# Optimization experiments

Measured on AMD Instinct MI355X. Metric: run time of the kernel, lower is better.

Reference implementation:

```python
import jax, jax.numpy as jnp
import numpy as np

N, E, IN, K, F, D = 50000, 800000, 256, 4, 64, 2


def setup_inputs() -> dict:
    key = jax.random.key(0)
    ks = jax.random.split(key, 10)
    # CSR rowptr: 0 .. E, nondecreasing, endpoints pinned
    inner = jnp.sort(jax.random.randint(ks[0], (N - 1,), 0, E + 1))
    rowptr = jnp.concatenate([jnp.zeros(1, jnp.int64), inner.astype(jnp.int64), jnp.full(1, E, jnp.int64)])
    colind = jax.random.randint(ks[1], (E,), 0, N).astype(jnp.int64)
    # CSC mirrors (used only by the fused kernel's backward; inert in forward math)
    inner_c = jnp.sort(jax.random.randint(ks[2], (N - 1,), 0, E + 1))
    colptr = jnp.concatenate([jnp.zeros(1, jnp.int64), inner_c.astype(jnp.int64), jnp.full(1, E, jnp.int64)])
    rowind = jax.random.randint(ks[3], (E,), 0, N).astype(jnp.int64)
    permute = jnp.arange(E, dtype=jnp.int64)
    feat = jax.random.normal(ks[4], (N, IN), dtype=jnp.float32)
    pseudo = jax.random.uniform(ks[5], (E, D), dtype=jnp.float32)
    # params: fc weight [K*F, IN] (xavier-normal style scale), mu ~ N(0, 0.1), inv_sigma = 1, bias = 0
    gain = float(np.sqrt(2.0))
    std = gain * float(np.sqrt(2.0 / (IN + K * F)))
    W_fc = jax.random.normal(ks[6], (K * F, IN), dtype=jnp.float32) * std
    mu = jax.random.normal(ks[7], (K, D), dtype=jnp.float32) * 0.1
    inv_sigma = jnp.ones((K, D), dtype=jnp.float32)
    bias = jnp.zeros((F,), dtype=jnp.float32)
    return {"rowptr": rowptr, "colind": colind, "colptr": colptr, "rowind": rowind,
            "permute": permute, "feat": feat, "pseudo": pseudo,
            "W_fc": W_fc, "mu": mu, "inv_sigma": inv_sigma, "bias": bias}


def reference(rowptr, colind, colptr, rowind, permute, feat, pseudo, W_fc, mu, inv_sigma, bias):
    n = feat.shape[0]
    e = colind.shape[0]
    k, d = mu.shape
    f = W_fc.shape[0] // k
    # dense projection: [N, K, F]
    node_feat = (feat @ W_fc.T).reshape(n, k, f)
    # per-edge Gaussian mixture weights: [E, K]
    diff = pseudo[:, None, :] - mu[None, :, :]              # [E, K, D]
    gaussian = jnp.exp(jnp.sum(-0.5 * diff * diff * (inv_sigma[None, :, :] ** 2), axis=-1))
    # multi-head SpMM: gather source feats, weight per kernel, sum kernels (sum commutes
    # with the segment reduction, so fold the head-sum into the edge message): [E, F]
    msg = jnp.einsum('ek,ekf->ef', gaussian, node_feat[colind])
    # destination node of each CSR edge
    dst = jnp.searchsorted(rowptr, jnp.arange(e), side='right') - 1
    rst = jax.ops.segment_sum(msg, dst, num_segments=n)      # [N, F]
    return rst + bias
```

## Files before the change

### kernel.cpp

```cpp
#include <hip/hip_runtime.h>


typedef _Float16 f16;
typedef __attribute__((ext_vector_type(2))) _Float16 f16x2;
typedef __attribute__((ext_vector_type(4))) _Float16 f16x4;
typedef __attribute__((ext_vector_type(8))) _Float16 f16x8;
typedef __attribute__((ext_vector_type(4))) float f32x4;

__device__ inline f16x4 cvt4h(float4 v) {
    f16x4 h;
    h.x = (f16)v.x; h.y = (f16)v.y; h.z = (f16)v.z; h.w = (f16)v.w;
    return h;
}

__global__ __launch_bounds__(256) void convert_W(
    const float* __restrict__ W, f16* __restrict__ Wp)
{
    const int gid = blockIdx.x * 256 + threadIdx.x;
    const int jp = gid >> 6, k4 = gid & 63;
    const int wrow = ((jp & 3) << 6) | (jp >> 2);
    reinterpret_cast<f16x4*>(Wp)[jp * 64 + k4] =
        cvt4h(reinterpret_cast<const float4*>(W)[wrow * 64 + k4]);
}

#define ASTRIDE 264

__global__ __launch_bounds__(256) void gemm_fused(
    const float* __restrict__ feat,
    const f16* __restrict__ Wp,
    f16* __restrict__ nf,
    int M)
{
    __shared__ f16 As[64 * ASTRIDE];
    __shared__ f16 Bs[256 * 32];
    const int t    = threadIdx.x;
    const int lane = t & 63;
    const int wave = t >> 6;
    const int bm   = blockIdx.x * 64;
    const int l16  = lane & 15;
    const int quad = lane >> 4;
    const int wn   = wave * 64;

    size_t bsrc[4];
#pragma unroll
    for (int j = 0; j < 4; ++j)
        bsrc[j] = (size_t)(wave * 64 + j * 16 + (lane >> 2)) * 256 + (lane & 3) * 8;

    typedef __attribute__((address_space(3))) void lds_t;
    typedef const __attribute__((address_space(1))) void gm_t;

#pragma unroll
    for (int j = 0; j < 4; ++j)
        __builtin_amdgcn_global_load_lds((gm_t*)(Wp + bsrc[j]),
            (lds_t*)(Bs + (wave * 4 + j) * 512), 16, 0, 0);

#pragma unroll
    for (int it = 0; it < 8; ++it) {
        const int flat = it * 2048 + t * 8;
        const int row  = flat >> 8;
        const int koff = flat & 255;
        const float* src = feat + (size_t)min(bm + row, M - 1) * 256 + koff;
        const float4 a0 = *reinterpret_cast<const float4*>(src);
        const float4 a1 = *reinterpret_cast<const float4*>(src + 4);
        *reinterpret_cast<f16x4*>(&As[row * ASTRIDE + koff])     = cvt4h(a0);
        *reinterpret_cast<f16x4*>(&As[row * ASTRIDE + koff + 4]) = cvt4h(a1);
    }

    f32x4 acc[4][4];
#pragma unroll
    for (int mi = 0; mi < 4; ++mi)
#pragma unroll
        for (int ni = 0; ni < 4; ++ni)
            acc[mi][ni] = (f32x4){0.f, 0.f, 0.f, 0.f};

    for (int ki = 0; ki < 8; ++ki) {
        __syncthreads();

        f16x8 af[4], bfr[4];
#pragma unroll
        for (int mi = 0; mi < 4; ++mi)
            af[mi] = *reinterpret_cast<const f16x8*>(
                &As[(mi * 16 + l16) * ASTRIDE + ki * 32 + quad * 8]);
#pragma unroll
        for (int ni = 0; ni < 4; ++ni)
            bfr[ni] = *reinterpret_cast<const f16x8*>(
                &Bs[(wn + ni * 16 + l16) * 32 + quad * 8]);

        __syncthreads();
        if (ki < 7) {
            const int k0 = (ki + 1) * 32;
#pragma unroll
            for (int j = 0; j < 4; ++j)
                __builtin_amdgcn_global_load_lds((gm_t*)(Wp + bsrc[j] + k0),
                    (lds_t*)(Bs + (wave * 4 + j) * 512), 16, 0, 0);
        }
#pragma unroll
        for (int mi = 0; mi < 4; ++mi)
#pragma unroll
            for (int ni = 0; ni < 4; ++ni)
                acc[mi][ni] = __builtin_amdgcn_mfma_f32_16x16x32_f16(
                    af[mi], bfr[ni], acc[mi][ni], 0, 0, 0);
    }

#pragma unroll
    for (int mi = 0; mi < 4; ++mi) {
#pragma unroll
        for (int r = 0; r < 4; ++r) {
            const int row = bm + mi * 16 + quad * 4 + r;
            if (row < M) {
#pragma unroll
                for (int ni = 0; ni < 4; ++ni) {
                    const int col = wn + ni * 16 + l16;
                    nf[(size_t)row * 256 + col] = (f16)(acc[mi][ni][r]);
                }
            }
        }
    }
}

__global__ __launch_bounds__(128) void edge_aggregate(
    const int* __restrict__ rowptr,
    const int* __restrict__ colind,
    const float* __restrict__ pseudo,
    const f16* __restrict__ nf,
    const float* __restrict__ mu,
    const float* __restrict__ inv_sigma,
    const float* __restrict__ bias,
    float* __restrict__ out,
    int N)
{
    __shared__ f16 gbuf[2][64];
    __shared__ int cbuf[2][16];
    const int wave = threadIdx.x >> 6;
    const int lane = threadIdx.x & 63;
    const int node = blockIdx.x * 2 + wave;
    if (node >= N) return;

    const int kk = lane >> 4;
    const int ii = lane & 15;
    const float mx = mu[2 * kk], my = mu[2 * kk + 1];
    const float sa = inv_sigma[2 * kk], sb = inv_sigma[2 * kk + 1];
    const float sx = sa * sa, sy = sb * sb;

    const int e0 = rowptr[node];
    const int e1 = rowptr[node + 1];
    f16* gw = gbuf[wave];
    int* cw = cbuf[wave];

    float a4[4] = {0.f, 0.f, 0.f, 0.f};
    for (int ec = e0; ec < e1; ec += 16) {
        const int cnt = min(16, e1 - ec);
        {
            const bool v = ii < cnt;
            const int e = v ? (ec + ii) : e0;
            const float2 p = *reinterpret_cast<const float2*>(pseudo + 2 * (size_t)e);
            const float dx = p.x - mx, dy = p.y - my;
            const float g = v ? __expf(-0.5f * (dx * dx * sx + dy * dy * sy)) : 0.f;
            gw[ii * 4 + kk] = (f16)g;
            if (kk == 0) cw[ii] = v ? colind[e] : 0;
        }
        __builtin_amdgcn_wave_barrier();
        __threadfence_block();
        const int cnt4 = (cnt + 3) & ~3;
        for (int i2 = 0; i2 < cnt4; i2 += 4) {
#pragma unroll
            for (int j = 0; j < 4; ++j) {
                const int c = cw[i2 + j];
                const f16x4 h = *reinterpret_cast<const f16x4*>(
                    nf + ((size_t)c << 8) + (lane << 2));
                const f16x2 g01 = *reinterpret_cast<const f16x2*>(&gw[(i2 + j) * 4]);
                const f16x2 g23 = *reinterpret_cast<const f16x2*>(&gw[(i2 + j) * 4 + 2]);
                const f16x2 h01 = __builtin_shufflevector(h, h, 0, 1);
                const f16x2 h23 = __builtin_shufflevector(h, h, 2, 3);
#if __has_builtin(__builtin_amdgcn_fdot2)
                a4[j] = __builtin_amdgcn_fdot2(h01, g01, a4[j], false);
                a4[j] = __builtin_amdgcn_fdot2(h23, g23, a4[j], false);
#else
                a4[j] += (float)h01.x * (float)g01.x + (float)h01.y * (float)g01.y
                       + (float)h23.x * (float)g23.x + (float)h23.y * (float)g23.y;
#endif
            }
        }
        __builtin_amdgcn_wave_barrier();
        __threadfence_block();
    }
    out[((size_t)node << 6) + lane] =
        (a4[0] + a4[1]) + (a4[2] + a4[3]) + bias[lane];
}

extern "C" void kernel_launch(void* const* d_in, const int* in_sizes, int n_in,
                              void* d_out, int out_size, void* d_ws, size_t ws_size,
                              hipStream_t stream)
{
    const int*   rowptr    = (const int*)d_in[0];
    const int*   colind    = (const int*)d_in[1];
    const float* feat      = (const float*)d_in[5];
    const float* pseudo    = (const float*)d_in[6];
    const float* W_fc      = (const float*)d_in[7];
    const float* mu        = (const float*)d_in[8];
    const float* inv_sigma = (const float*)d_in[9];
    const float* bias      = (const float*)d_in[10];
    float* out = (float*)d_out;

    const int N = in_sizes[0] - 1;
    f16* nf = (f16*)d_ws;
    f16* Wp = (f16*)d_out;

    hipLaunchKernelGGL(convert_W, dim3(64), dim3(256), 0, stream, W_fc, Wp);

    hipLaunchKernelGGL(gemm_fused, dim3((N + 63) / 64), dim3(256), 0, stream,
                       feat, Wp, nf, N);

    hipLaunchKernelGGL(edge_aggregate, dim3((N + 1) / 2), dim3(128), 0, stream,
                       rowptr, colind, pseudo, nf, mu, inv_sigma, bias, out, N);
}
```

Before: 189.6 us.

## Quantize projected node features and gaussian weights to int8 with per-row scales

The GEMM epilogue now quantizes each node's projected features to int8 with one scale per row and per head, staging the result through shared memory for coalesced stores. The edge aggregation gathers int8 rows plus scales and uses an int8 dot4 against gaussian weights quantized to int8. The goal is to halve the gather bytes in the memory-bound SpMM phase. In exchange it loses accuracy and adds a scale load per edge.

```diff
diff --git a/kernel.cpp b/kernel.cpp
--- a/kernel.cpp
+++ b/kernel.cpp
@@ -2,7 +2,6 @@
 
 
 typedef _Float16 f16;
-typedef __attribute__((ext_vector_type(2))) _Float16 f16x2;
 typedef __attribute__((ext_vector_type(4))) _Float16 f16x4;
 typedef __attribute__((ext_vector_type(8))) _Float16 f16x8;
 typedef __attribute__((ext_vector_type(4))) float f32x4;
@@ -11,6 +10,17 @@
     f16x4 h;
     h.x = (f16)v.x; h.y = (f16)v.y; h.z = (f16)v.z; h.w = (f16)v.w;
     return h;
+}
+
+__device__ inline int dot4_i8(int a, int b) {
+#if __has_builtin(__builtin_amdgcn_sdot4)
+    return __builtin_amdgcn_sdot4(a, b, 0, false);
+#else
+    return (int)(char)(a)       * (int)(char)(b)
+         + (int)(char)(a >> 8)  * (int)(char)(b >> 8)
+         + (int)(char)(a >> 16) * (int)(char)(b >> 16)
+         + (int)(char)(a >> 24) * (int)(char)(b >> 24);
+#endif
 }
 
 __global__ __launch_bounds__(256) void convert_W(
@@ -24,15 +34,19 @@
 }
 
 #define ASTRIDE 264
+#define AS_BYTES (64 * ASTRIDE * 2)
 
 __global__ __launch_bounds__(256) void gemm_fused(
     const float* __restrict__ feat,
     const f16* __restrict__ Wp,
-    f16* __restrict__ nf,
+    char* __restrict__ nfq,
+    float* __restrict__ sc,
     int M)
 {
-    __shared__ f16 As[64 * ASTRIDE];
-    __shared__ f16 Bs[256 * 32];
+    __shared__ char smem[AS_BYTES + 256 * 32 * 2];
+    f16* As = (f16*)smem;
+    f16* Bs = (f16*)(smem + AS_BYTES);
+    char* qt = smem + AS_BYTES;
     const int t    = threadIdx.x;
     const int lane = t & 63;
     const int wave = t >> 6;
@@ -106,14 +120,37 @@
     for (int mi = 0; mi < 4; ++mi) {
 #pragma unroll
         for (int r = 0; r < 4; ++r) {
-            const int row = bm + mi * 16 + quad * 4 + r;
-            if (row < M) {
-#pragma unroll
-                for (int ni = 0; ni < 4; ++ni) {
-                    const int col = wn + ni * 16 + l16;
-                    nf[(size_t)row * 256 + col] = (f16)(acc[mi][ni][r]);
-                }
+            float am = 0.f;
+#pragma unroll
+            for (int ni = 0; ni < 4; ++ni)
+                am = fmaxf(am, fabsf(acc[mi][ni][r]));
+            am = fmaxf(am, __shfl_xor(am, 1));
+            am = fmaxf(am, __shfl_xor(am, 2));
+            am = fmaxf(am, __shfl_xor(am, 4));
+            am = fmaxf(am, __shfl_xor(am, 8));
+            const float sinv = am > 0.f ? 127.f / am : 0.f;
+            const int rl = mi * 16 + quad * 4 + r;
+#pragma unroll
+            for (int ni = 0; ni < 4; ++ni)
+                qt[rl * 256 + wn + ni * 16 + l16] =
+                    (char)(int)__builtin_rintf(acc[mi][ni][r] * sinv);
+            if (l16 == 0) {
+                const int row = bm + rl;
+                if (row < M) sc[row * 4 + wave] = am * (1.f / 16129.f);
             }
+        }
+    }
+    __syncthreads();
+
+    {
+        const int rl  = t >> 2;
+        const int co  = (t & 3) * 64;
+        const int row = bm + rl;
+        if (row < M) {
+            const int4* s4 = reinterpret_cast<const int4*>(qt + rl * 256 + co);
+            int4* d4 = reinterpret_cast<int4*>(nfq + (size_t)row * 256 + co);
+#pragma unroll
+            for (int j = 0; j < 4; ++j) d4[j] = s4[j];
         }
     }
 }
@@ -122,14 +159,15 @@
     const int* __restrict__ rowptr,
     const int* __restrict__ colind,
     const float* __restrict__ pseudo,
-    const f16* __restrict__ nf,
+    const char* __restrict__ nfq,
+    const float* __restrict__ sc,
     const float* __restrict__ mu,
     const float* __restrict__ inv_sigma,
     const float* __restrict__ bias,
     float* __restrict__ out,
     int N)
 {
-    __shared__ f16 gbuf[2][64];
+    __shared__ int gpack[2][16];
     __shared__ int cbuf[2][16];
     const int wave = threadIdx.x >> 6;
     const int lane = threadIdx.x & 63;
@@ -144,7 +182,7 @@
 
     const int e0 = rowptr[node];
     const int e1 = rowptr[node + 1];
-    f16* gw = gbuf[wave];
+    int* gp = gpack[wave];
     int* cw = cbuf[wave];
 
     float a4[4] = {0.f, 0.f, 0.f, 0.f};
@@ -156,7 +194,7 @@
             const float2 p = *reinterpret_cast<const float2*>(pseudo + 2 * (size_t)e);
             const float dx = p.x - mx, dy = p.y - my;
             const float g = v ? __expf(-0.5f * (dx * dx * sx + dy * dy * sy)) : 0.f;
-            gw[ii * 4 + kk] = (f16)g;
+            ((char*)&gp[ii])[kk] = (char)(int)(g * 127.f + 0.5f);
             if (kk == 0) cw[ii] = v ? colind[e] : 0;
         }
         __builtin_amdgcn_wave_barrier();
@@ -166,19 +204,11 @@
 #pragma unroll
             for (int j = 0; j < 4; ++j) {
                 const int c = cw[i2 + j];
-                const f16x4 h = *reinterpret_cast<const f16x4*>(
-                    nf + ((size_t)c << 8) + (lane << 2));
-                const f16x2 g01 = *reinterpret_cast<const f16x2*>(&gw[(i2 + j) * 4]);
-                const f16x2 g23 = *reinterpret_cast<const f16x2*>(&gw[(i2 + j) * 4 + 2]);
-                const f16x2 h01 = __builtin_shufflevector(h, h, 0, 1);
-                const f16x2 h23 = __builtin_shufflevector(h, h, 2, 3);
-#if __has_builtin(__builtin_amdgcn_fdot2)
-                a4[j] = __builtin_amdgcn_fdot2(h01, g01, a4[j], false);
-                a4[j] = __builtin_amdgcn_fdot2(h23, g23, a4[j], false);
-#else
-                a4[j] += (float)h01.x * (float)g01.x + (float)h01.y * (float)g01.y
-                       + (float)h23.x * (float)g23.x + (float)h23.y * (float)g23.y;
-#endif
+                const int q = *reinterpret_cast<const int*>(
+                    nfq + ((size_t)c << 8) + (lane << 2));
+                const float s = sc[c * 4 + (lane >> 4)];
+                const int d = dot4_i8(q, gp[i2 + j]);
+                a4[j] += s * (float)d;
             }
         }
         __builtin_amdgcn_wave_barrier();
@@ -203,14 +233,15 @@
     float* out = (float*)d_out;
 
     const int N = in_sizes[0] - 1;
-    f16* nf = (f16*)d_ws;
-    f16* Wp = (f16*)d_out;
+    char*  nfq = (char*)d_ws;
+    float* sc  = (float*)(nfq + (size_t)N * 256);
+    f16*   Wp  = (f16*)d_out;
 
     hipLaunchKernelGGL(convert_W, dim3(64), dim3(256), 0, stream, W_fc, Wp);
 
     hipLaunchKernelGGL(gemm_fused, dim3((N + 63) / 64), dim3(256), 0, stream,
-                       feat, Wp, nf, N);
+                       feat, Wp, nfq, sc, N);
 
     hipLaunchKernelGGL(edge_aggregate, dim3((N + 1) / 2), dim3(128), 0, stream,
-                       rowptr, colind, pseudo, nf, mu, inv_sigma, bias, out, N);
-}
+                       rowptr, colind, pseudo, nfq, sc, mu, inv_sigma, bias, out, N);
+}
```

Result: faster. 182.6 us (-3.7%).
